# Kernel tuning notes

Hardware: AMD Instinct MI355X
Metric: run time of the kernel (lower is better)

## Reference

```python
import jax, jax.numpy as jnp
import numpy as np

BLOCKSIZE = 4096
OUT_FEATURES = 16384
IN_FEATURES = 4096
BATCH, SEQ = 4, 2048


def setup_inputs() -> dict:
    key = jax.random.key(0)
    k_x, k_w, k_a, k_b = jax.random.split(key, 4)
    x = jax.random.normal(k_x, (BATCH, SEQ, IN_FEATURES), dtype=jnp.float32)
    # quantized int8 weight stored as indices into the 256-entry codebook
    weight_q = jax.random.randint(k_w, (OUT_FEATURES, IN_FEATURES), 0, 256, dtype=jnp.int32)
    n_blocks = (OUT_FEATURES * IN_FEATURES) // BLOCKSIZE  # 16384
    absmax = jax.random.uniform(k_a, (n_blocks,), dtype=jnp.float32) + 0.5
    # bitsandbytes dynamic-map code: a sorted table of values in [-1, 1]
    code = jnp.linspace(-1.0, 1.0, 256, dtype=jnp.float32)
    bias = jax.random.normal(k_b, (OUT_FEATURES,), dtype=jnp.float32) * 0.02
    return {"x": x, "weight_q": weight_q, "absmax": absmax, "code": code, "bias": bias}


def dequantize_blockwise(weight_q, absmax, code):
    # codebook lookup then per-block absmax scaling
    flat = code[weight_q.reshape(-1)]                      # [out*in]
    flat = flat.reshape(-1, BLOCKSIZE) * absmax[:, None]   # [n_blocks, blocksize]
    return flat.reshape(weight_q.shape)                    # [out, in]


def reference(x, weight_q, absmax, code, bias):
    w = dequantize_blockwise(weight_q, absmax, code)       # [out, in] fp32
    # F.linear(x, w, bias) = x @ w.T + bias
    return jnp.einsum("bsi,oi->bso", x, w) + bias
```

## Files before the change

kernel.cpp:

```cpp
#include <hip/hip_runtime.h>
#include <hip/hip_bf16.h>
#include <stdint.h>

#define M_TOTAL 8192
#define N_TOTAL 16384
#define K_TOTAL 4096

#define BM 256
#define BN 256
#define BK 64
#define NKT (K_TOTAL / BK)

using f32x16 = __attribute__((ext_vector_type(16))) float;
using bf16x8 = __attribute__((ext_vector_type(8))) short;

#define UNROLL _Pragma("unroll")

__device__ __forceinline__ unsigned short f2bf(float f) {
    union { float f; unsigned u; } v; v.f = f;
    unsigned r = v.u + 0x7fffu + ((v.u >> 16) & 1u);
    return (unsigned short)(r >> 16);
}

__device__ __forceinline__ void gload_lds16(const void* g, void* l) {
    __builtin_amdgcn_global_load_lds(
        (const __attribute__((address_space(1))) unsigned int*)g,
        (__attribute__((address_space(3))) unsigned int*)l,
        16, 0, 0);
}

__global__ void dequant_w_kernel(const int* __restrict__ q,
                                 const float* __restrict__ am,
                                 const float* __restrict__ code,
                                 unsigned short* __restrict__ wb) {
    __shared__ float lc[256];
    if (threadIdx.x < 256) lc[threadIdx.x] = code[threadIdx.x];
    __syncthreads();
    const int total = (N_TOTAL / 4) * K_TOTAL;
    const int stride = gridDim.x * blockDim.x;
    for (int i = blockIdx.x * blockDim.x + threadIdx.x; i < total; i += stride) {
        int4 v = reinterpret_cast<const int4*>(q)[i];
        float a = am[i >> 10];
        ushort4 o;
        o.x = f2bf(lc[v.x & 255] * a);
        o.y = f2bf(lc[v.y & 255] * a);
        o.z = f2bf(lc[v.z & 255] * a);
        o.w = f2bf(lc[v.w & 255] * a);
        reinterpret_cast<ushort4*>(wb)[i] = o;
    }
}

__global__ void cvt_x_kernel(const float* __restrict__ x,
                             unsigned short* __restrict__ xb) {
    const int total = (M_TOTAL * K_TOTAL) / 4;
    const int stride = gridDim.x * blockDim.x;
    for (int i = blockIdx.x * blockDim.x + threadIdx.x; i < total; i += stride) {
        float4 v = reinterpret_cast<const float4*>(x)[i];
        ushort4 o;
        o.x = f2bf(v.x); o.y = f2bf(v.y); o.z = f2bf(v.z); o.w = f2bf(v.w);
        reinterpret_cast<ushort4*>(xb)[i] = o;
    }
}

__global__ __launch_bounds__(256, 1) void gemm_bw_kernel(
        const unsigned short* __restrict__ A,
        const unsigned short* __restrict__ B,
        const float* __restrict__ bias,
        float* __restrict__ C) {
    __shared__ __align__(16) unsigned short sA[2][BM * BK];
    __shared__ __align__(16) unsigned short sB[2][BN * BK];

    const int nwg = gridDim.x;
    const int bid = blockIdx.x;
    const int wg  = (bid & 7) * (nwg >> 3) + (bid >> 3);
    const int nbn = N_TOTAL / BN;
    const int brow = (wg / nbn) * BM;
    const int bcol = (wg % nbn) * BN;

    const int tid  = threadIdx.x;
    const int wid  = tid >> 6;
    const int lane = tid & 63;
    const int wm   = wid >> 1;
    const int wn   = wid & 1;

    const int srow = wid * 8 + (lane >> 3);
    const int scol = ((lane & 7) ^ (lane >> 3)) * 8;
    const unsigned short* Asrc = A + (long long)(brow + srow) * K_TOTAL + scol;
    const unsigned short* Bsrc = B + (long long)(bcol + srow) * K_TOTAL + scol;

    auto stA = [&](int i, int kt, int b) {
        gload_lds16(Asrc + (long long)(i * 32) * K_TOTAL + kt * BK,
                    &sA[b][(i * 32 + wid * 8) * BK]);
    };
    auto stB = [&](int i, int kt, int b) {
        gload_lds16(Bsrc + (long long)(i * 32) * K_TOTAL + kt * BK,
                    &sB[b][(i * 32 + wid * 8) * BK]);
    };
    auto stage_tile = [&](int kt, int b) {
        UNROLL for (int i = 0; i < 8; ++i) stA(i, kt, b);
        UNROLL for (int i = 0; i < 8; ++i) stB(i, kt, b);
    };

    const int l31 = lane & 31;
    const int l7  = lane & 7;
    const int kh  = lane >> 5;

    f32x16 acc[4][4];
    UNROLL for (int mf = 0; mf < 4; ++mf)
        UNROLL for (int nf = 0; nf < 4; ++nf)
            UNROLL for (int r = 0; r < 16; ++r)
                acc[mf][nf][r] = 0.f;

#define COMPUTE(P)                                                                \
    UNROLL for (int ks = 0; ks < 4; ++ks) {                                       \
        bf16x8 af[4], bf[4];                                                      \
        UNROLL for (int mf = 0; mf < 4; ++mf) {                                   \
            const int row = wm * 128 + mf * 32 + l31;                             \
            af[mf] = *reinterpret_cast<const bf16x8*>(                            \
                &sA[P][row * BK + (((ks * 2 + kh) ^ l7) * 8)]);                   \
        }                                                                         \
        UNROLL for (int nf = 0; nf < 4; ++nf) {                                   \
            const int row = wn * 128 + nf * 32 + l31;                             \
            bf[nf] = *reinterpret_cast<const bf16x8*>(                            \
                &sB[P][row * BK + (((ks * 2 + kh) ^ l7) * 8)]);                   \
        }                                                                         \
        UNROLL for (int mf = 0; mf < 4; ++mf)                                     \
            UNROLL for (int nf = 0; nf < 4; ++nf)                                 \
                acc[mf][nf] = __builtin_amdgcn_mfma_f32_32x32x16_bf16(            \
                    af[mf], bf[nf], acc[mf][nf], 0, 0, 0);                        \
    }

#define GATEV()                                                                   \
    asm volatile("s_waitcnt lgkmcnt(0) vmcnt(0)" ::: "memory");                   \
    __builtin_amdgcn_s_barrier();                                                 \
    asm volatile("" ::: "memory");

    stage_tile(0, 0);
    GATEV();

    for (int it = 0; it < NKT / 2 - 1; ++it) {
        stage_tile(2 * it + 1, 1);
        COMPUTE(0)
        GATEV();
        stage_tile(2 * it + 2, 0);
        COMPUTE(1)
        GATEV();
    }
    stage_tile(NKT - 1, 1);
    COMPUTE(0)
    GATEV();
    COMPUTE(1)

    UNROLL for (int mf = 0; mf < 4; ++mf)
        UNROLL for (int nf = 0; nf < 4; ++nf) {
            const int col = bcol + wn * 128 + nf * 32 + l31;
            const float bv = bias[col];
            const long long rbase = (long long)brow + wm * 128 + mf * 32 + 4 * kh;
            UNROLL for (int r = 0; r < 16; ++r) {
                const long long row = rbase + (r & 3) + 8 * (r >> 2);
                C[row * N_TOTAL + col] = acc[mf][nf][r] + bv;
            }
        }
}

extern "C" void kernel_launch(void* const* d_in, const int* in_sizes, int n_in,
                              void* d_out, int out_size, void* d_ws, size_t ws_size,
                              hipStream_t stream) {
    const float* x      = (const float*)d_in[0];
    const int*   wq     = (const int*)  d_in[1];
    const float* absmax = (const float*)d_in[2];
    const float* code   = (const float*)d_in[3];
    const float* bias   = (const float*)d_in[4];
    float* out = (float*)d_out;

    unsigned short* wb = (unsigned short*)d_ws;
    unsigned short* xb = wb + (size_t)N_TOTAL * K_TOTAL;

    dequant_w_kernel<<<2048, 256, 0, stream>>>(wq, absmax, code, wb);
    cvt_x_kernel   <<<2048, 256, 0, stream>>>(x, xb);

    dim3 grid((M_TOTAL / BM) * (N_TOTAL / BN));
    gemm_bw_kernel<<<grid, 256, 0, stream>>>(xb, wb, bias, out);
}
```

Before: 1.332 ms.

## Use 16 waves per block with 16x16x32 MFMA tiles and setprio

The GEMM block grows from 4 to 16 waves (1024 threads) in a 4x4 wave grid, each wave computing a 64x64 sub-tile with 16x16x32 bf16 MFMAs in place of 32x32x16. Global-to-LDS staging is spread across the extra waves, and s_setprio raises priority around the MFMA bursts. The aim is more latency hiding and better overlap of LDS reads with MFMA work. In exchange, each wave does less reuse per LDS fragment and 16 waves must meet at every barrier.

Result: faster. 1.099 ms (-17.4%).

```diff
diff --git a/kernel.cpp b/kernel.cpp
--- a/kernel.cpp
+++ b/kernel.cpp
@@ -11,7 +11,7 @@
 #define BK 64
 #define NKT (K_TOTAL / BK)
 
-using f32x16 = __attribute__((ext_vector_type(16))) float;
+using f32x4  = __attribute__((ext_vector_type(4))) float;
 using bf16x8 = __attribute__((ext_vector_type(8))) short;
 
 #define UNROLL _Pragma("unroll")
@@ -62,7 +62,7 @@
     }
 }
 
-__global__ __launch_bounds__(256, 1) void gemm_bw_kernel(
+__global__ __launch_bounds__(1024, 1) void gemm_w16_kernel(
         const unsigned short* __restrict__ A,
         const unsigned short* __restrict__ B,
         const float* __restrict__ bias,
@@ -80,87 +80,84 @@
     const int tid  = threadIdx.x;
     const int wid  = tid >> 6;
     const int lane = tid & 63;
-    const int wm   = wid >> 1;
-    const int wn   = wid & 1;
+    const int wm   = wid >> 2;
+    const int wn   = wid & 3;
 
     const int srow = wid * 8 + (lane >> 3);
     const int scol = ((lane & 7) ^ (lane >> 3)) * 8;
     const unsigned short* Asrc = A + (long long)(brow + srow) * K_TOTAL + scol;
     const unsigned short* Bsrc = B + (long long)(bcol + srow) * K_TOTAL + scol;
 
-    auto stA = [&](int i, int kt, int b) {
-        gload_lds16(Asrc + (long long)(i * 32) * K_TOTAL + kt * BK,
-                    &sA[b][(i * 32 + wid * 8) * BK]);
-    };
-    auto stB = [&](int i, int kt, int b) {
-        gload_lds16(Bsrc + (long long)(i * 32) * K_TOTAL + kt * BK,
-                    &sB[b][(i * 32 + wid * 8) * BK]);
-    };
-    auto stage_tile = [&](int kt, int b) {
-        UNROLL for (int i = 0; i < 8; ++i) stA(i, kt, b);
-        UNROLL for (int i = 0; i < 8; ++i) stB(i, kt, b);
+    auto stage = [&](int kt, int b) {
+        UNROLL for (int j = 0; j < 2; ++j)
+            gload_lds16(Asrc + (long long)(j * 128) * K_TOTAL + kt * BK,
+                        &sA[b][(j * 128 + wid * 8) * BK]);
+        UNROLL for (int j = 0; j < 2; ++j)
+            gload_lds16(Bsrc + (long long)(j * 128) * K_TOTAL + kt * BK,
+                        &sB[b][(j * 128 + wid * 8) * BK]);
     };
 
-    const int l31 = lane & 31;
-    const int l7  = lane & 7;
-    const int kh  = lane >> 5;
+    const int arow_base = wm * 64 + (lane & 15);
+    const int brow_base = wn * 64 + (lane & 15);
+    const int rslot_hi  = lane >> 4;
+    const int rslot_xor = lane & 7;
 
-    f32x16 acc[4][4];
+    f32x4 acc[4][4];
     UNROLL for (int mf = 0; mf < 4; ++mf)
         UNROLL for (int nf = 0; nf < 4; ++nf)
-            UNROLL for (int r = 0; r < 16; ++r)
-                acc[mf][nf][r] = 0.f;
+            acc[mf][nf] = (f32x4){0.f, 0.f, 0.f, 0.f};
 
 #define COMPUTE(P)                                                                \
-    UNROLL for (int ks = 0; ks < 4; ++ks) {                                       \
-        bf16x8 af[4], bf[4];                                                      \
-        UNROLL for (int mf = 0; mf < 4; ++mf) {                                   \
-            const int row = wm * 128 + mf * 32 + l31;                             \
-            af[mf] = *reinterpret_cast<const bf16x8*>(                            \
-                &sA[P][row * BK + (((ks * 2 + kh) ^ l7) * 8)]);                   \
-        }                                                                         \
-        UNROLL for (int nf = 0; nf < 4; ++nf) {                                   \
-            const int row = wn * 128 + nf * 32 + l31;                             \
-            bf[nf] = *reinterpret_cast<const bf16x8*>(                            \
-                &sB[P][row * BK + (((ks * 2 + kh) ^ l7) * 8)]);                   \
-        }                                                                         \
+    UNROLL for (int ks = 0; ks < 2; ++ks) {                                       \
+        bf16x8 a4[4], b4[4];                                                      \
+        UNROLL for (int mf = 0; mf < 4; ++mf)                                     \
+            a4[mf] = *reinterpret_cast<const bf16x8*>(                            \
+                &sA[P][(arow_base + mf * 16) * BK +                               \
+                       (((ks * 4 + rslot_hi) ^ rslot_xor) * 8)]);                 \
+        UNROLL for (int nf = 0; nf < 4; ++nf)                                     \
+            b4[nf] = *reinterpret_cast<const bf16x8*>(                            \
+                &sB[P][(brow_base + nf * 16) * BK +                               \
+                       (((ks * 4 + rslot_hi) ^ rslot_xor) * 8)]);                 \
+        __builtin_amdgcn_s_setprio(1);                                            \
         UNROLL for (int mf = 0; mf < 4; ++mf)                                     \
             UNROLL for (int nf = 0; nf < 4; ++nf)                                 \
-                acc[mf][nf] = __builtin_amdgcn_mfma_f32_32x32x16_bf16(            \
-                    af[mf], bf[nf], acc[mf][nf], 0, 0, 0);                        \
+                acc[mf][nf] = __builtin_amdgcn_mfma_f32_16x16x32_bf16(            \
+                    a4[mf], b4[nf], acc[mf][nf], 0, 0, 0);                        \
+        __builtin_amdgcn_s_setprio(0);                                            \
     }
 
-#define GATEV()                                                                   \
+#define GATE()                                                                    \
     asm volatile("s_waitcnt lgkmcnt(0) vmcnt(0)" ::: "memory");                   \
     __builtin_amdgcn_s_barrier();                                                 \
     asm volatile("" ::: "memory");
 
-    stage_tile(0, 0);
-    GATEV();
+    stage(0, 0);
+    GATE();
 
     for (int it = 0; it < NKT / 2 - 1; ++it) {
-        stage_tile(2 * it + 1, 1);
+        stage(2 * it + 1, 1);
         COMPUTE(0)
-        GATEV();
-        stage_tile(2 * it + 2, 0);
+        GATE();
+        stage(2 * it + 2, 0);
         COMPUTE(1)
-        GATEV();
+        GATE();
     }
-    stage_tile(NKT - 1, 1);
+    stage(63, 1);
     COMPUTE(0)
-    GATEV();
+    GATE();
     COMPUTE(1)
 
-    UNROLL for (int mf = 0; mf < 4; ++mf)
+    const int crow0 = (lane >> 4) * 4;
+    const int ccol  = lane & 15;
+    UNROLL for (int mf = 0; mf < 4; ++mf) {
+        const long long row0 = (long long)brow + wm * 64 + mf * 16 + crow0;
         UNROLL for (int nf = 0; nf < 4; ++nf) {
-            const int col = bcol + wn * 128 + nf * 32 + l31;
+            const int col = bcol + wn * 64 + nf * 16 + ccol;
             const float bv = bias[col];
-            const long long rbase = (long long)brow + wm * 128 + mf * 32 + 4 * kh;
-            UNROLL for (int r = 0; r < 16; ++r) {
-                const long long row = rbase + (r & 3) + 8 * (r >> 2);
-                C[row * N_TOTAL + col] = acc[mf][nf][r] + bv;
-            }
+            UNROLL for (int r = 0; r < 4; ++r)
+                C[(row0 + r) * N_TOTAL + col] = acc[mf][nf][r] + bv;
         }
+    }
 }
 
 extern "C" void kernel_launch(void* const* d_in, const int* in_sizes, int n_in,
@@ -180,5 +177,5 @@
     cvt_x_kernel   <<<2048, 256, 0, stream>>>(x, xb);
 
     dim3 grid((M_TOTAL / BM) * (N_TOTAL / BN));
-    gemm_bw_kernel<<<grid, 256, 0, stream>>>(xb, wb, bias, out);
+    gemm_w16_kernel<<<grid, 1024, 0, stream>>>(xb, wb, bias, out);
 }
```
